# Kernel optimization log

Hardware: AMD Instinct MI355X
Metric: run time of the kernel (lower is better)

## Reference

```python
import jax, jax.numpy as jnp
import numpy as np

MAX_SHIFT = 15            # sampling_rate // 2 with sampling_rate = 30
NUM_SHIFTS = 2 * MAX_SHIFT + 1


def setup_inputs() -> dict:
    key = jax.random.key(0)
    k1, k2, k3, k4 = jax.random.split(key, 4)
    B, T, P = 128, 16384, 32
    y_pred = jax.random.normal(k1, (B, T), dtype=jnp.float32)
    y_true = jax.random.normal(k2, (B, T), dtype=jnp.float32)
    # theta_s: per-participant latent shift logits (init 1/S in torch; random here)
    theta = jax.random.normal(k3, (P, NUM_SHIFTS), dtype=jnp.float32) * 0.1
    participant_idx = jax.random.randint(k4, (B,), 0, P, dtype=jnp.int32)
    return {"y_pred": y_pred, "y_true": y_true, "theta": theta,
            "participant_idx": participant_idx}


def reference(y_pred, y_true, theta, participant_idx):
    # y_pred, y_true: [B, T]; theta: [P, S]; participant_idx: [B]
    B, T = y_pred.shape
    M = MAX_SHIFT
    S = NUM_SHIFTS
    # Zero-pad both sides; slice start M+shift reproduces the torch pad logic
    # for both negative and positive shifts (out-of-range values are 0).
    padded = jnp.pad(y_true, ((0, 0), (M, M)))              # [B, T+2M]
    idx = jnp.arange(S)[:, None] + jnp.arange(T)[None, :]   # [S, T]
    shifted = padded[:, idx]                                # [B, S, T]
    mse_per_shift = jnp.mean((y_pred[:, None, :] - shifted) ** 2, axis=-1)  # [B, S]
    # training path: participant-wise softmax mixture over shifts
    p_k = jax.nn.softmax(theta[participant_idx], axis=-1)   # [B, S]
    return jnp.mean(jnp.sum(mse_per_shift * p_k, axis=-1))
```

## Files before the change

### kernel.cpp

```cpp
#include <hip/hip_runtime.h>
#include <math.h>

#define T_LEN 16384
#define B_N   128
#define S_N   31
#define M_SH  15
#define NCHUNK 8
#define TCHUNK (T_LEN / NCHUNK)
#define BLOCK  256
#define VT     8
#define NBLOCKS (B_N * NCHUNK)
#define HALO   16
#define TILE_F4 ((TCHUNK + 2 * HALO) / 4)

__device__ __forceinline__ int swz(int f4) { return f4 ^ ((f4 >> 3) & 7); }

__global__ __launch_bounds__(BLOCK) void talos_main(
    const float* __restrict__ y_pred,
    const float* __restrict__ y_true,
    const float* __restrict__ theta,
    const int* __restrict__ pidx,
    float* __restrict__ accp,
    float* __restrict__ sqp) {

  __shared__ float tile[TILE_F4 * 4];
  __shared__ float wsh[S_N];
  __shared__ float redL[BLOCK / 64], redS[BLOCK / 64];

  const int bid   = blockIdx.x;
  const int b     = bid / NCHUNK;
  const int chunk = bid % NCHUNK;
  const int t0    = chunk * TCHUNK;
  const int tid   = threadIdx.x;
  const float* yt_b = y_true + b * T_LEN;
  const float* yp_b = y_pred + b * T_LEN;

  for (int f = tid; f < TILE_F4; f += BLOCK) {
    int g = t0 - HALO + f * 4;
    float4 v;
    if (g >= 0 && g + 3 < T_LEN) {
      v = *(const float4*)(yt_b + g);
    } else {
      v.x = (g + 0 >= 0 && g + 0 < T_LEN) ? yt_b[g + 0] : 0.f;
      v.y = (g + 1 >= 0 && g + 1 < T_LEN) ? yt_b[g + 1] : 0.f;
      v.z = (g + 2 >= 0 && g + 2 < T_LEN) ? yt_b[g + 2] : 0.f;
      v.w = (g + 3 >= 0 && g + 3 < T_LEN) ? yt_b[g + 3] : 0.f;
    }
    *(float4*)&tile[swz(f) * 4] = v;
  }

  if (tid < 32) {
    float v = (tid < S_N) ? theta[pidx[b] * S_N + tid] : -1e30f;
    float m = v;
#pragma unroll
    for (int off = 16; off; off >>= 1) m = fmaxf(m, __shfl_xor(m, off, 32));
    float e = (tid < S_N) ? __expf(v - m) : 0.f;
    float s = e;
#pragma unroll
    for (int off = 16; off; off >>= 1) s += __shfl_xor(s, off, 32);
    if (tid < S_N) wsh[tid] = e / s;
  }
  __syncthreads();

  const int lt0 = tid * VT;
  float yp[VT];
  *(float4*)&yp[0] = *(const float4*)(yp_b + t0 + lt0);
  *(float4*)&yp[4] = *(const float4*)(yp_b + t0 + lt0 + 4);

  float win[VT + 2 * HALO];
#pragma unroll
  for (int q = 0; q < (VT + 2 * HALO) / 4; ++q) {
    int f4 = (lt0 >> 2) + q;
    *(float4*)&win[q * 4] = *(const float4*)&tile[swz(f4) * 4];
  }

  float w[S_N];
#pragma unroll
  for (int s = 0; s < S_N; ++s) w[s] = wsh[s];

  float lin[VT];
#pragma unroll
  for (int j = 0; j < VT; ++j) lin[j] = 0.f;
#pragma unroll
  for (int s = 0; s < S_N; ++s) {
#pragma unroll
    for (int j = 0; j < VT; ++j)
      lin[j] = fmaf(w[s], win[j + s + 1], lin[j]);
  }

  float accL = 0.f, accS = 0.f;
#pragma unroll
  for (int j = 0; j < VT; ++j) {
    accL = fmaf(yp[j], fmaf(-2.f, lin[j], yp[j]), accL);
    float a = win[HALO + j];
    accS = fmaf(a, a, accS);
  }

#pragma unroll
  for (int off = 32; off; off >>= 1) {
    accL += __shfl_down(accL, off, 64);
    accS += __shfl_down(accS, off, 64);
  }
  const int lane = tid & 63, wv = tid >> 6;
  if (lane == 0) { redL[wv] = accL; redS[wv] = accS; }
  __syncthreads();
  if (tid == 0) {
    float sL = 0.f, sS = 0.f;
#pragma unroll
    for (int i = 0; i < BLOCK / 64; ++i) { sL += redL[i]; sS += redS[i]; }
    accp[bid] = sL;
    sqp[bid]  = sS;
  }
}

__global__ __launch_bounds__(128) void talos_final(
    const float* __restrict__ y_true,
    const float* __restrict__ theta,
    const int* __restrict__ pidx,
    const float* __restrict__ accp,
    const float* __restrict__ sqp,
    float* __restrict__ out) {
  __shared__ double red[2];
  const int b = threadIdx.x;

  double A = 0.0, S = 0.0;
  for (int c = 0; c < NCHUNK; ++c) {
    A += (double)accp[b * NCHUNK + c];
    S += (double)sqp[b * NCHUNK + c];
  }

  const float* th = theta + pidx[b] * S_N;
  float v[S_N];
  float m = -1e30f;
#pragma unroll
  for (int s = 0; s < S_N; ++s) { v[s] = th[s]; m = fmaxf(m, v[s]); }
  float sum = 0.f;
#pragma unroll
  for (int s = 0; s < S_N; ++s) { v[s] = __expf(v[s] - m); sum += v[s]; }
  const float inv = 1.f / sum;

  const float* yt = y_true + b * T_LEN;
  float pf[M_SH + 1], sf[M_SH + 1];
  pf[0] = 0.f; sf[0] = 0.f;
  for (int i = 1; i <= M_SH; ++i) {
    float a = yt[i - 1];        pf[i] = pf[i - 1] + a * a;
    float z = yt[T_LEN - i];    sf[i] = sf[i - 1] + z * z;
  }

  double sq = 0.0;
  for (int s = 0; s < S_N; ++s) {
    int k = s - M_SH;
    float edge = (k >= 0) ? pf[k] : sf[-k];
    sq += (double)(v[s] * inv) * (S - (double)edge);
  }

  double loss = A + sq;
#pragma unroll
  for (int off = 32; off; off >>= 1) loss += __shfl_down(loss, off, 64);
  if ((b & 63) == 0) red[b >> 6] = loss;
  __syncthreads();
  if (b == 0) out[0] = (float)((red[0] + red[1]) / ((double)T_LEN * (double)B_N));
}

extern "C" void kernel_launch(void* const* d_in, const int* in_sizes, int n_in,
                              void* d_out, int out_size, void* d_ws, size_t ws_size,
                              hipStream_t stream) {
  const float* y_pred = (const float*)d_in[0];
  const float* y_true = (const float*)d_in[1];
  const float* theta  = (const float*)d_in[2];
  const int*   pidx   = (const int*)d_in[3];
  float* out = (float*)d_out;

  float* accp = (float*)d_ws;
  float* sqp  = accp + NBLOCKS;

  talos_main<<<NBLOCKS, BLOCK, 0, stream>>>(y_pred, y_true, theta, pidx, accp, sqp);
  talos_final<<<1, 128, 0, stream>>>(y_true, theta, pidx, accp, sqp, out);
}
```

Before: 12.78 us.

## Fuse final reduction into main kernel via last-block atomic ticket

Removes the separate finalize kernel. Each block now folds the squared-norm term and the boundary edge corrections into a single partial, and the last block to take an atomic ticket sums all partials and writes the output. This saves a kernel launch and its dependency gap. In exchange it adds a hipMemsetAsync, an atomic with threadfence per block, and a serial tail in the last block.

```diff
diff --git a/kernel.cpp b/kernel.cpp
--- a/kernel.cpp
+++ b/kernel.cpp
@@ -20,12 +20,14 @@
     const float* __restrict__ y_true,
     const float* __restrict__ theta,
     const int* __restrict__ pidx,
-    float* __restrict__ accp,
-    float* __restrict__ sqp) {
+    float* __restrict__ partial,
+    unsigned int* __restrict__ ticket,
+    float* __restrict__ out) {
 
   __shared__ float tile[TILE_F4 * 4];
   __shared__ float wsh[S_N];
-  __shared__ float redL[BLOCK / 64], redS[BLOCK / 64];
+  __shared__ float redL[BLOCK / 64];
+  __shared__ int   is_last;
 
   const int bid   = blockIdx.x;
   const int b     = bid / NCHUNK;
@@ -74,92 +76,77 @@
     *(float4*)&win[q * 4] = *(const float4*)&tile[swz(f4) * 4];
   }
 
-  float w[S_N];
-#pragma unroll
-  for (int s = 0; s < S_N; ++s) w[s] = wsh[s];
-
   float lin[VT];
 #pragma unroll
   for (int j = 0; j < VT; ++j) lin[j] = 0.f;
 #pragma unroll
   for (int s = 0; s < S_N; ++s) {
+    const float ws = wsh[s];
 #pragma unroll
     for (int j = 0; j < VT; ++j)
-      lin[j] = fmaf(w[s], win[j + s + 1], lin[j]);
+      lin[j] = fmaf(ws, win[j + s + 1], lin[j]);
   }
 
-  float accL = 0.f, accS = 0.f;
+  float acc = 0.f;
 #pragma unroll
   for (int j = 0; j < VT; ++j) {
-    accL = fmaf(yp[j], fmaf(-2.f, lin[j], yp[j]), accL);
+    acc = fmaf(yp[j], fmaf(-2.f, lin[j], yp[j]), acc);
     float a = win[HALO + j];
-    accS = fmaf(a, a, accS);
+    acc = fmaf(a, a, acc);
   }
 
 #pragma unroll
-  for (int off = 32; off; off >>= 1) {
-    accL += __shfl_down(accL, off, 64);
-    accS += __shfl_down(accS, off, 64);
+  for (int off = 32; off; off >>= 1) acc += __shfl_down(acc, off, 64);
+  const int lane = tid & 63, wv = tid >> 6;
+  if (lane == 0) redL[wv] = acc;
+  __syncthreads();
+
+  if (tid == 0) {
+    float P = 0.f;
+#pragma unroll
+    for (int i = 0; i < BLOCK / 64; ++i) P += redL[i];
+
+    if (chunk == 0) {
+      float pf = 0.f, corr = 0.f;
+      for (int k = 1; k <= M_SH; ++k) {
+        float a = yt_b[k - 1]; pf = fmaf(a, a, pf);
+        corr = fmaf(wsh[k + M_SH], pf, corr);
+      }
+      P -= corr;
+    }
+    if (chunk == NCHUNK - 1) {
+      float sf = 0.f, corr = 0.f;
+      for (int j = 1; j <= M_SH; ++j) {
+        float z = yt_b[T_LEN - j]; sf = fmaf(z, z, sf);
+        corr = fmaf(wsh[M_SH - j], sf, corr);
+      }
+      P -= corr;
+    }
+
+    partial[bid] = P;
+    __threadfence();
+    unsigned int t = atomicAdd(ticket, 1u);
+    is_last = (t == NBLOCKS - 1);
   }
-  const int lane = tid & 63, wv = tid >> 6;
-  if (lane == 0) { redL[wv] = accL; redS[wv] = accS; }
   __syncthreads();
-  if (tid == 0) {
-    float sL = 0.f, sS = 0.f;
+
+  if (is_last) {
+    __threadfence();
+    volatile const float* vp = partial;
+    double a = 0.0;
+    for (int i = tid; i < NBLOCKS; i += BLOCK) a += (double)vp[i];
 #pragma unroll
-    for (int i = 0; i < BLOCK / 64; ++i) { sL += redL[i]; sS += redS[i]; }
-    accp[bid] = sL;
-    sqp[bid]  = sS;
+    for (int off = 32; off; off >>= 1) a += __shfl_down(a, off, 64);
+    __shared__ double redD[BLOCK / 64];
+    if (lane == 0) redD[wv] = a;
+    __syncthreads();
+    if (tid == 0) {
+      double tot = 0.0;
+#pragma unroll
+      for (int i = 0; i < BLOCK / 64; ++i) tot += redD[i];
+      out[0] = (float)(tot / ((double)T_LEN * (double)B_N));
+    }
   }
-}
-
-__global__ __launch_bounds__(128) void talos_final(
-    const float* __restrict__ y_true,
-    const float* __restrict__ theta,
-    const int* __restrict__ pidx,
-    const float* __restrict__ accp,
-    const float* __restrict__ sqp,
-    float* __restrict__ out) {
-  __shared__ double red[2];
-  const int b = threadIdx.x;
-
-  double A = 0.0, S = 0.0;
-  for (int c = 0; c < NCHUNK; ++c) {
-    A += (double)accp[b * NCHUNK + c];
-    S += (double)sqp[b * NCHUNK + c];
-  }
-
-  const float* th = theta + pidx[b] * S_N;
-  float v[S_N];
-  float m = -1e30f;
-#pragma unroll
-  for (int s = 0; s < S_N; ++s) { v[s] = th[s]; m = fmaxf(m, v[s]); }
-  float sum = 0.f;
-#pragma unroll
-  for (int s = 0; s < S_N; ++s) { v[s] = __expf(v[s] - m); sum += v[s]; }
-  const float inv = 1.f / sum;
-
-  const float* yt = y_true + b * T_LEN;
-  float pf[M_SH + 1], sf[M_SH + 1];
-  pf[0] = 0.f; sf[0] = 0.f;
-  for (int i = 1; i <= M_SH; ++i) {
-    float a = yt[i - 1];        pf[i] = pf[i - 1] + a * a;
-    float z = yt[T_LEN - i];    sf[i] = sf[i - 1] + z * z;
-  }
-
-  double sq = 0.0;
-  for (int s = 0; s < S_N; ++s) {
-    int k = s - M_SH;
-    float edge = (k >= 0) ? pf[k] : sf[-k];
-    sq += (double)(v[s] * inv) * (S - (double)edge);
-  }
-
-  double loss = A + sq;
-#pragma unroll
-  for (int off = 32; off; off >>= 1) loss += __shfl_down(loss, off, 64);
-  if ((b & 63) == 0) red[b >> 6] = loss;
-  __syncthreads();
-  if (b == 0) out[0] = (float)((red[0] + red[1]) / ((double)T_LEN * (double)B_N));
 }
 
 extern "C" void kernel_launch(void* const* d_in, const int* in_sizes, int n_in,
@@ -171,9 +158,10 @@
   const int*   pidx   = (const int*)d_in[3];
   float* out = (float*)d_out;
 
-  float* accp = (float*)d_ws;
-  float* sqp  = accp + NBLOCKS;
+  float*        partial = (float*)d_ws;
+  unsigned int* ticket  = (unsigned int*)((char*)d_ws + 4096);
 
-  talos_main<<<NBLOCKS, BLOCK, 0, stream>>>(y_pred, y_true, theta, pidx, accp, sqp);
-  talos_final<<<1, 128, 0, stream>>>(y_true, theta, pidx, accp, sqp, out);
+  hipMemsetAsync(ticket, 0, sizeof(unsigned int), stream);
+  talos_main<<<NBLOCKS, BLOCK, 0, stream>>>(y_pred, y_true, theta, pidx,
+                                            partial, ticket, out);
 }
```

Result: slower. 35.58 us (+178.5%).
